# Kernel optimization log

Measured on AMD Instinct MI355X. Metric: run time of the kernel, lower is better.

Reference implementation:

```python
import jax, jax.numpy as jnp
import numpy as np

N, E = 100000, 1600000
NFEAT, NHID, NCLASS = 128, 128, 40


def _glorot(key, shape):
    lim = float(np.sqrt(6.0 / (shape[0] + shape[1])))
    return jax.random.uniform(key, shape, jnp.float32, -lim, lim)


def setup_inputs() -> dict:
    key = jax.random.key(0)
    ks = jax.random.split(key, 9)
    x = jax.random.normal(ks[0], (N, NFEAT), jnp.float32)
    edge_index = jax.random.randint(ks[1], (2, E), 0, N, jnp.int32)
    return {
        "x": x,
        "edge_index": edge_index,
        # layer 1: lin_l (aggregated, with bias) and lin_r (root, no bias)
        "W1l": _glorot(ks[2], (NFEAT, NHID)), "b1": jnp.zeros((NHID,), jnp.float32),
        "W1r": _glorot(ks[3], (NFEAT, NHID)),
        "W2l": _glorot(ks[4], (NHID, NHID)), "b2": jnp.zeros((NHID,), jnp.float32),
        "W2r": _glorot(ks[5], (NHID, NHID)),
        "W3l": _glorot(ks[6], (NHID, NCLASS)), "b3": jnp.zeros((NCLASS,), jnp.float32),
        "W3r": _glorot(ks[7], (NHID, NCLASS)),
    }


def _sage_conv(x, src, dst, Wl, bl, Wr):
    # mean-aggregate source features at destination nodes (PyG SAGEConv, aggr='mean')
    msg = x[src]                                                  # [E, d] gather
    agg = jax.ops.segment_sum(msg, dst, num_segments=N)           # [N, d] scatter-add
    deg = jax.ops.segment_sum(jnp.ones((src.shape[0], 1), x.dtype), dst, num_segments=N)
    mean = agg / jnp.maximum(deg, 1.0)
    return mean @ Wl + bl + x @ Wr


def reference(x, edge_index, W1l, b1, W1r, W2l, b2, W2r, W3l, b3, W3r):
    src, dst = edge_index[0], edge_index[1]
    h = jax.nn.relu(_sage_conv(x, src, dst, W1l, b1, W1r))
    # dropout is identity in eval mode (training=False)
    h = jax.nn.relu(_sage_conv(h, src, dst, W2l, b2, W2r))
    embeddings = h
    logits = _sage_conv(h, src, dst, W3l, b3, W3r)
    return jax.nn.log_softmax(logits, axis=1), embeddings
```

## Files before the change

kernel.cpp:

```cpp
#include <hip/hip_runtime.h>
#include <math.h>

#define NCLASS 40
#define BEDG 1024
#define CAP 24576

typedef float f32x4 __attribute__((ext_vector_type(4)));
typedef __bf16 bf16x8 __attribute__((ext_vector_type(8)));

typedef __attribute__((address_space(1))) const void gv_t;
typedef __attribute__((address_space(3))) void lv_t;
#define GLOAD_LDS16(g, l) __builtin_amdgcn_global_load_lds((gv_t*)(g), (lv_t*)(l), 16, 0, 0)
#define NTL(p) __builtin_nontemporal_load(p)

__device__ inline unsigned short f2bf(float f) {
  unsigned u = __float_as_uint(f);
  unsigned r = (u + 0x7fff + ((u >> 16) & 1)) >> 16;
  return (unsigned short)r;
}
__device__ inline float bflo(unsigned v) { return __uint_as_float(v << 16); }
__device__ inline float bfhi(unsigned v) { return __uint_as_float(v & 0xffff0000u); }


__global__ void k_bcount(const int* __restrict__ dst, int E, int PART,
                         int* __restrict__ bcnt) {
  __shared__ int lc[8];
  int k = blockIdx.x;
  if (threadIdx.x < 8) lc[threadIdx.x] = 0;
  __syncthreads();
  int lo = k * BEDG, hi = min(lo + BEDG, E);
  for (int i = lo + threadIdx.x; i < hi; i += blockDim.x)
    atomicAdd(&lc[NTL(&dst[i]) / PART], 1);
  __syncthreads();
  if (threadIdx.x < 8) bcnt[k * 8 + threadIdx.x] = lc[threadIdx.x];
}

__global__ void k_bscanA(int* __restrict__ bcnt, int nbB, int* __restrict__ btot) {
  __shared__ int tmp[256];
  __shared__ int carryS;
  int b = blockIdx.x;
  int tid = threadIdx.x;
  if (tid == 0) carryS = 0;
  __syncthreads();
  for (int c0 = 0; c0 < nbB; c0 += 256) {
    int idx = c0 + tid;
    int v = (idx < nbB) ? bcnt[idx * 8 + b] : 0;
    tmp[tid] = v;
    __syncthreads();
    for (int d = 1; d < 256; d <<= 1) {
      int t = (tid >= d) ? tmp[tid - d] : 0;
      __syncthreads();
      tmp[tid] += t;
      __syncthreads();
    }
    if (idx < nbB) bcnt[idx * 8 + b] = carryS + tmp[tid] - v;
    __syncthreads();
    if (tid == 255) carryS += tmp[255];
    __syncthreads();
  }
  if (tid == 0) btot[b] = carryS;
}

__global__ void k_bbase(const int* __restrict__ btot, int* __restrict__ bbase) {
  if (threadIdx.x == 0) {
    int s = 0;
    for (int b = 0; b < 8; ++b) {
      bbase[b] = s;
      s += btot[b];
    }
    bbase[8] = s;
  }
}

__global__ void k_place(const int* __restrict__ dst, const int* __restrict__ src, int E,
                        int PART, const int* __restrict__ bcnt,
                        const int* __restrict__ bbase, int* __restrict__ ebuf) {
  __shared__ int lbase[8];
  __shared__ int lcnt[8];
  int k = blockIdx.x;
  if (threadIdx.x < 8) {
    lbase[threadIdx.x] = bbase[threadIdx.x] + bcnt[k * 8 + threadIdx.x];
    lcnt[threadIdx.x] = 0;
  }
  __syncthreads();
  int lo = k * BEDG, hi = min(lo + BEDG, E);
  for (int i = lo + threadIdx.x; i < hi; i += blockDim.x) {
    int d = NTL(&dst[i]);
    int s = NTL(&src[i]);
    int p = d / PART;
    int r = atomicAdd(&lcnt[p], 1);
    ebuf[lbase[p] + r] = (int)(((unsigned)(d - p * PART) << 17) | (unsigned)s);
  }
}

__global__ void k_bcount2(const int* __restrict__ ebuf, const int* __restrict__ bbase,
                          int CB, int* __restrict__ bcnt2) {
  __shared__ int lc[32];
  int p = blockIdx.x & 7, j = blockIdx.x >> 3;
  int tid = threadIdx.x;
  if (tid < 32) lc[tid] = 0;
  __syncthreads();
  int lo = bbase[p], hi = bbase[p + 1];
  for (int base = lo + j * BEDG; base < hi; base += CB * BEDG) {
    int end = min(base + BEDG, hi);
    for (int i = base + tid; i < end; i += 256)
      atomicAdd(&lc[(((unsigned)NTL(&ebuf[i])) >> 17) >> 9], 1);
  }
  __syncthreads();
  if (tid < 32) bcnt2[(p * CB + j) * 32 + tid] = lc[tid];
}

__global__ void k_bscan2(int* __restrict__ bcnt2, int CB, int* __restrict__ tot2) {
  __shared__ int tmp[256];
  int p = blockIdx.x >> 5, k = blockIdx.x & 31;
  int tid = threadIdx.x;
  int v = (tid < CB) ? bcnt2[(p * CB + tid) * 32 + k] : 0;
  tmp[tid] = v;
  __syncthreads();
  for (int d = 1; d < 256; d <<= 1) {
    int t = (tid >= d) ? tmp[tid - d] : 0;
    __syncthreads();
    tmp[tid] += t;
    __syncthreads();
  }
  if (tid < CB) bcnt2[(p * CB + tid) * 32 + k] = tmp[tid] - v;
  if (tid == 255) tot2[p * 32 + k] = tmp[255];
}

__global__ void k_base2(const int* __restrict__ bbase, const int* __restrict__ tot2,
                        int* __restrict__ base2) {
  int p = threadIdx.x;
  if (p >= 8) return;
  int s = bbase[p];
  for (int k = 0; k < 32; ++k) {
    base2[p * 32 + k] = s;
    s += tot2[p * 32 + k];
  }
}

__global__ void k_place2(const int* __restrict__ ebuf, const int* __restrict__ bbase,
                         const int* __restrict__ bcnt2, const int* __restrict__ base2,
                         int CB, int* __restrict__ ebuf2) {
  __shared__ int lb[32];
  int p = blockIdx.x & 7, j = blockIdx.x >> 3;
  int tid = threadIdx.x;
  if (tid < 32) lb[tid] = base2[p * 32 + tid] + bcnt2[(p * CB + j) * 32 + tid];
  __syncthreads();
  int lo = bbase[p], hi = bbase[p + 1];
  for (int base = lo + j * BEDG; base < hi; base += CB * BEDG) {
    int end = min(base + BEDG, hi);
    for (int i = base + tid; i < end; i += 256) {
      unsigned pk = (unsigned)NTL(&ebuf[i]);
      int pos = atomicAdd(&lb[(pk >> 17) >> 9], 1);
      ebuf2[pos] = (int)pk;
    }
  }
}

__global__ __launch_bounds__(256) void k_csr(const int* __restrict__ ebuf2,
                                             const int* __restrict__ base2,
                                             const int* __restrict__ tot2, int PART,
                                             int N, int E, int* __restrict__ off,
                                             int* __restrict__ col) {
  __shared__ int cnt[512];
  __shared__ int cur[512];
  __shared__ int tmp[256];
  __shared__ int stage[CAP];
  int p = blockIdx.x & 7, k = blockIdx.x >> 3;
  int tid = threadIdx.x;
  if (p == 0 && k == 0 && tid == 0) off[N] = E;
  int n0l = k << 9;
  if (n0l >= PART) return;
  int node0 = p * PART + n0l;
  if (node0 >= N) return;
  int nn = min(512, PART - n0l);
  nn = min(nn, N - node0);
  int lo = base2[p * 32 + k];
  int tot = tot2[p * 32 + k];

  cnt[tid] = 0;
  cnt[tid + 256] = 0;
  __syncthreads();
  for (int i = lo + tid; i < lo + tot; i += 256)
    atomicAdd(&cnt[(((unsigned)ebuf2[i]) >> 17) & 511], 1);
  __syncthreads();

  int v0 = cnt[2 * tid], v1 = cnt[2 * tid + 1];
  int s = v0 + v1;
  tmp[tid] = s;
  __syncthreads();
  for (int d = 1; d < 256; d <<= 1) {
    int t = (tid >= d) ? tmp[tid - d] : 0;
    __syncthreads();
    tmp[tid] += t;
    __syncthreads();
  }
  int excl = tmp[tid] - s;
  cnt[2 * tid] = excl;
  cnt[2 * tid + 1] = excl + v0;
  cur[2 * tid] = excl;
  cur[2 * tid + 1] = excl + v0;
  __syncthreads();

  for (int i = tid; i < nn; i += 256) off[node0 + i] = lo + cnt[i];

  if (tot <= CAP) {
    for (int i = lo + tid; i < lo + tot; i += 256) {
      unsigned pk = (unsigned)ebuf2[i];
      int pos = atomicAdd(&cur[(pk >> 17) & 511], 1);
      stage[pos] = (int)(pk & 0x1FFFFu);
    }
    __syncthreads();
    for (int i = tid; i < tot; i += 256) col[lo + i] = stage[i];
  } else {
    for (int i = lo + tid; i < lo + tot; i += 256) {
      unsigned pk = (unsigned)ebuf2[i];
      int pos = atomicAdd(&cur[(pk >> 17) & 511], 1);
      col[lo + pos] = (int)(pk & 0x1FFFFu);
    }
  }
}

__global__ void k_cast(const float4* __restrict__ x, uint4* __restrict__ xb, int n8) {
  int i = blockIdx.x * blockDim.x + threadIdx.x;
  if (i >= n8) return;
  float4 a = x[i * 2], b = x[i * 2 + 1];
  uint4 o;
  o.x = (unsigned)f2bf(a.x) | ((unsigned)f2bf(a.y) << 16);
  o.y = (unsigned)f2bf(a.z) | ((unsigned)f2bf(a.w) << 16);
  o.z = (unsigned)f2bf(b.x) | ((unsigned)f2bf(b.y) << 16);
  o.w = (unsigned)f2bf(b.z) | ((unsigned)f2bf(b.w) << 16);
  xb[i] = o;
}

__global__ void k_prepw(const float* __restrict__ W1l, const float* __restrict__ W1r,
                        const float* __restrict__ W2l, const float* __restrict__ W2r,
                        const float* __restrict__ W3l, const float* __restrict__ W3r,
                        unsigned short* __restrict__ Wth1, unsigned short* __restrict__ Wth2,
                        unsigned short* __restrict__ Wth3) {
  int idx = blockIdx.x * blockDim.x + threadIdx.x;
  if (idx < 32768) {
    int h = idx >> 14, c = (idx >> 7) & 127, k = idx & 127;
    const float* W = h ? W1r : W1l;
    Wth1[idx] = f2bf(W[k * 128 + c]);
  } else if (idx < 65536) {
    int j = idx - 32768;
    int h = j >> 14, c = (j >> 7) & 127, k = j & 127;
    const float* W = h ? W2r : W2l;
    Wth2[j] = f2bf(W[k * 128 + c]);
  } else if (idx < 65536 + 16384) {
    int j = idx - 65536;
    int h = j >> 13, c = (j >> 7) & 63, k = j & 127;
    float v = 0.f;
    if (c < NCLASS) v = (h ? W3r : W3l)[k * NCLASS + c];
    Wth3[j] = f2bf(v);
  }
}

#define ACC8(u, sc)                          \
  acc[0] = fmaf(bflo(u.x), sc, acc[0]);      \
  acc[1] = fmaf(bfhi(u.x), sc, acc[1]);      \
  acc[2] = fmaf(bflo(u.y), sc, acc[2]);      \
  acc[3] = fmaf(bfhi(u.y), sc, acc[3]);      \
  acc[4] = fmaf(bflo(u.z), sc, acc[4]);      \
  acc[5] = fmaf(bfhi(u.z), sc, acc[5]);      \
  acc[6] = fmaf(bflo(u.w), sc, acc[6]);      \
  acc[7] = fmaf(bfhi(u.w), sc, acc[7]);

__global__ void k_aggb(const char* __restrict__ X, const int* __restrict__ off,
                       const int* __restrict__ col, int n, uint4* __restrict__ out) {
  int wid = (blockIdx.x * blockDim.x + threadIdx.x) >> 6;
  int lane = threadIdx.x & 63;
  if (wid >= n) return;
  int g = lane >> 4, q = lane & 15;
  unsigned qb = (unsigned)q << 4;
  int s = off[wid], e = off[wid + 1];
  float acc[8];
#pragma unroll
  for (int t = 0; t < 8; ++t) acc[t] = 0.f;
  int e1 = e - 1;
  for (int j = s; j < e; j += 8) {
    int i0 = j + g, i1 = i0 + 4;
    int c0 = NTL(&col[min(i0, e1)]);
    int c1 = NTL(&col[min(i1, e1)]);
    float s0 = (i0 < e) ? 1.f : 0.f;
    float s1 = (i1 < e) ? 1.f : 0.f;
    uint4 u0 = *(const uint4*)(X + (((unsigned)c0 << 8) + qb));
    uint4 u1 = *(const uint4*)(X + (((unsigned)c1 << 8) + qb));
    ACC8(u0, s0);
    ACC8(u1, s1);
  }
#pragma unroll
  for (int t = 0; t < 8; ++t) {
    acc[t] += __shfl_xor(acc[t], 16);
    acc[t] += __shfl_xor(acc[t], 32);
  }
  float inv = 1.0f / fmaxf((float)(e - s), 1.0f);
  uint4 o;
  o.x = (unsigned)f2bf(acc[0] * inv) | ((unsigned)f2bf(acc[1] * inv) << 16);
  o.y = (unsigned)f2bf(acc[2] * inv) | ((unsigned)f2bf(acc[3] * inv) << 16);
  o.z = (unsigned)f2bf(acc[4] * inv) | ((unsigned)f2bf(acc[5] * inv) << 16);
  o.w = (unsigned)f2bf(acc[6] * inv) | ((unsigned)f2bf(acc[7] * inv) << 16);
  if (lane < 16) out[(size_t)wid * 16 + lane] = o;
}

template <int COLS, int HALVES, int EPI>
__global__ __launch_bounds__(256) void k_gemm_mfma(
    const unsigned short* __restrict__ Aagg, const unsigned short* __restrict__ Aroot,
    const unsigned short* __restrict__ Wth, const float* __restrict__ bias, int n,
    float* __restrict__ outF, unsigned short* __restrict__ outB) {
  constexpr int RF = 4;
  constexpr int CF = 4;
  __shared__ unsigned short aS[128 * 128];
  __shared__ unsigned short wS[COLS * 128];
  int tid = threadIdx.x;
  int w = tid >> 6, lane = tid & 63, l15 = lane & 15, kg = lane >> 4;
  int rowBase = blockIdx.x * 128;
  int r0 = (w >> 1) * 64;
  int c0 = (w & 1) * 64;

  f32x4 acc[RF][CF];
#pragma unroll
  for (int i = 0; i < RF; ++i)
#pragma unroll
    for (int j = 0; j < CF; ++j) acc[i][j] = (f32x4){0.f, 0.f, 0.f, 0.f};

#pragma unroll
  for (int half = 0; half < HALVES; ++half) {
    if (half) __syncthreads();
    {
      const unsigned short* As = half ? Aroot : Aagg;
#pragma unroll
      for (int it = 0; it < 8; ++it) {
        int row = it * 16 + (tid >> 4);
        int g = rowBase + row;
        g = (g < n) ? g : (n - 1);
        int cb = (tid & 15) << 4;
        int sb = cb ^ ((row & 7) << 4);
        const char* src = (const char*)(As + (size_t)g * 128) + sb;
        char* dst = (char*)aS + it * 4096 + (tid >> 6) * 1024;
        GLOAD_LDS16(src, dst);
      }
      const unsigned short* Ws = Wth + (size_t)half * COLS * 128;
#pragma unroll
      for (int it = 0; it < COLS / 16; ++it) {
        int c = it * 16 + (tid >> 4);
        int cb = (tid & 15) << 4;
        int sb = cb ^ ((c & 7) << 4);
        const char* src = (const char*)(Ws + (size_t)c * 128) + sb;
        char* dst = (char*)wS + it * 4096 + (tid >> 6) * 1024;
        GLOAD_LDS16(src, dst);
      }
      asm volatile("s_waitcnt vmcnt(0)" ::: "memory");
      __syncthreads();
    }
#pragma unroll
    for (int ks = 0; ks < 4; ++ks) {
      int kb = ks * 64 + kg * 16;
      bf16x8 av[RF], bv[CF];
#pragma unroll
      for (int i = 0; i < RF; ++i) {
        int row = r0 + i * 16 + l15;
        av[i] = *(const bf16x8*)((const char*)aS + row * 256 + (kb ^ ((row & 7) << 4)));
      }
#pragma unroll
      for (int j = 0; j < CF; ++j) {
        int c = c0 + j * 16 + l15;
        bv[j] = *(const bf16x8*)((const char*)wS + c * 256 + (kb ^ ((c & 7) << 4)));
      }
#pragma unroll
      for (int i = 0; i < RF; ++i)
#pragma unroll
        for (int j = 0; j < CF; ++j)
          acc[i][j] = __builtin_amdgcn_mfma_f32_16x16x32_bf16(av[i], bv[j], acc[i][j], 0, 0, 0);
    }
  }

  if (EPI == 3) {
    bool leftHalf = (c0 == 0);
    unsigned short* R3b = (unsigned short*)outF;
    float bcol[CF];
#pragma unroll
    for (int j = 0; j < CF; ++j) {
      int c = c0 + j * 16 + l15;
      bcol[j] = (!leftHalf && (c - 64) < NCLASS) ? bias[c - 64] : 0.f;
    }
#pragma unroll
    for (int i = 0; i < RF; ++i) {
#pragma unroll
      for (int r = 0; r < 4; ++r) {
        int row = rowBase + r0 + i * 16 + kg * 4 + r;
        if (row >= n) continue;
#pragma unroll
        for (int j = 0; j < CF; ++j) {
          int c = c0 + j * 16 + l15;
          if (leftHalf) {
            outB[(size_t)row * 64 + c] = f2bf(acc[i][j][r]);
          } else {
            R3b[(size_t)row * 64 + (c - 64)] = f2bf(acc[i][j][r] + bcol[j]);
          }
        }
      }
    }
  } else {
    float bcol[CF];
#pragma unroll
    for (int j = 0; j < CF; ++j) bcol[j] = bias[c0 + j * 16 + l15];
#pragma unroll
    for (int i = 0; i < RF; ++i) {
#pragma unroll
      for (int r = 0; r < 4; ++r) {
        int row = rowBase + r0 + i * 16 + kg * 4 + r;
        if (row >= n) continue;
#pragma unroll
        for (int j = 0; j < CF; ++j) {
          float v = fmaxf(acc[i][j][r] + bcol[j], 0.f);
          int c = c0 + j * 16 + l15;
          outB[(size_t)row * 128 + c] = f2bf(v);
          if (EPI == 1) outF[(size_t)row * 128 + c] = v;
        }
      }
    }
  }
}

__global__ void k_agg3ls(const char* __restrict__ Y3, const char* __restrict__ R3,
                         const int* __restrict__ off, const int* __restrict__ col, int n,
                         float* __restrict__ out) {
  int wid = (blockIdx.x * blockDim.x + threadIdx.x) >> 6;
  int lane = threadIdx.x & 63;
  if (wid >= n) return;
  int g = lane >> 3, q = lane & 7;
  unsigned qb = (unsigned)q << 4;
  int s = off[wid], e = off[wid + 1];
  float acc[8];
#pragma unroll
  for (int t = 0; t < 8; ++t) acc[t] = 0.f;
  int e1 = e - 1;
  for (int j = s; j < e; j += 16) {
    int i0 = j + g, i1 = i0 + 8;
    int c0 = NTL(&col[min(i0, e1)]);
    int c1 = NTL(&col[min(i1, e1)]);
    float s0 = (i0 < e) ? 1.f : 0.f;
    float s1 = (i1 < e) ? 1.f : 0.f;
    uint4 u0 = *(const uint4*)(Y3 + (((unsigned)c0 << 7) + qb));
    uint4 u1 = *(const uint4*)(Y3 + (((unsigned)c1 << 7) + qb));
    ACC8(u0, s0);
    ACC8(u1, s1);
  }
#pragma unroll
  for (int t = 0; t < 8; ++t) {
    acc[t] += __shfl_xor(acc[t], 8);
    acc[t] += __shfl_xor(acc[t], 16);
    acc[t] += __shfl_xor(acc[t], 32);
  }
  float inv = 1.0f / fmaxf((float)(e - s), 1.0f);
  uint4 ur = *(const uint4*)(R3 + (((unsigned)wid << 7) + qb));
  float v[8];
  v[0] = acc[0] * inv + bflo(ur.x);
  v[1] = acc[1] * inv + bfhi(ur.x);
  v[2] = acc[2] * inv + bflo(ur.y);
  v[3] = acc[3] * inv + bfhi(ur.y);
  v[4] = acc[4] * inv + bflo(ur.z);
  v[5] = acc[5] * inv + bfhi(ur.z);
  v[6] = acc[6] * inv + bflo(ur.w);
  v[7] = acc[7] * inv + bfhi(ur.w);
  bool valid = q < 5;
  float m = -INFINITY;
  if (valid) {
#pragma unroll
    for (int t = 0; t < 8; ++t) m = fmaxf(m, v[t]);
  }
  m = fmaxf(m, __shfl_xor(m, 1));
  m = fmaxf(m, __shfl_xor(m, 2));
  m = fmaxf(m, __shfl_xor(m, 4));
  float sum = 0.f;
  if (valid) {
#pragma unroll
    for (int t = 0; t < 8; ++t) sum += expf(v[t] - m);
  }
  sum += __shfl_xor(sum, 1);
  sum += __shfl_xor(sum, 2);
  sum += __shfl_xor(sum, 4);
  float ls = logf(sum);
  if (lane < 5) {
    float4 o0 = make_float4(v[0] - m - ls, v[1] - m - ls, v[2] - m - ls, v[3] - m - ls);
    float4 o1 = make_float4(v[4] - m - ls, v[5] - m - ls, v[6] - m - ls, v[7] - m - ls);
    float* op = out + (size_t)wid * NCLASS + lane * 8;
    *(float4*)op = o0;
    *(float4*)(op + 4) = o1;
  }
}

extern "C" void kernel_launch(void* const* d_in, const int* in_sizes, int n_in,
                              void* d_out, int out_size, void* d_ws, size_t ws_size,
                              hipStream_t stream) {
  const float* x = (const float*)d_in[0];
  const int* ei = (const int*)d_in[1];
  const float* W1l = (const float*)d_in[2];
  const float* b1 = (const float*)d_in[3];
  const float* W1r = (const float*)d_in[4];
  const float* W2l = (const float*)d_in[5];
  const float* b2 = (const float*)d_in[6];
  const float* W2r = (const float*)d_in[7];
  const float* W3l = (const float*)d_in[8];
  const float* b3 = (const float*)d_in[9];
  const float* W3r = (const float*)d_in[10];

  int N = in_sizes[0] / 128;
  int E = in_sizes[1] / 2;
  const int* src = ei;
  const int* dst = ei + E;
  int PART = (N + 7) / 8;
  int nbB = (E + BEDG - 1) / BEDG;
  int CB = (E + 8 * BEDG - 1) / (8 * BEDG);
  if (CB > 256) CB = 256;
  if (CB < 1) CB = 1;

  char* wptr = (char*)d_ws;
  auto alloc = [&](size_t bytes) {
    void* p = (void*)wptr;
    wptr += (bytes + 255) & ~(size_t)255;
    return p;
  };
  int* off = (int*)alloc((size_t)(N + 1) * 4);
  int* col = (int*)alloc((size_t)E * 4);
  int* bcnt = (int*)alloc((size_t)nbB * 8 * 4);
  int* btot = (int*)alloc(16 * 4);
  int* bbase = (int*)alloc(16 * 4);
  int* bcnt2 = (int*)alloc((size_t)8 * CB * 32 * 4);
  int* tot2 = (int*)alloc(256 * 4);
  int* base2 = (int*)alloc(256 * 4);
  unsigned short* Wth1 = (unsigned short*)alloc(32768 * 2);
  unsigned short* Wth2 = (unsigned short*)alloc(32768 * 2);
  unsigned short* Wth3 = (unsigned short*)alloc(16384 * 2);
  unsigned short* xb = (unsigned short*)alloc((size_t)N * 128 * 2);
  unsigned short* mb = (unsigned short*)alloc((size_t)N * 128 * 2);
  unsigned short* h1 = (unsigned short*)alloc((size_t)N * 128 * 2);
  unsigned short* h2 = (unsigned short*)alloc((size_t)N * 128 * 2);

  float* outLS = (float*)d_out;
  float* emb = (float*)d_out + (size_t)N * NCLASS;

  int* ebuf = (int*)h2;
  int* ebuf2 = (int*)h2 + E;
  unsigned short* Y3 = mb;
  unsigned short* R3b = h1;

  k_bcount<<<nbB, 256, 0, stream>>>(dst, E, PART, bcnt);
  k_bscanA<<<8, 256, 0, stream>>>(bcnt, nbB, btot);
  k_bbase<<<1, 64, 0, stream>>>(btot, bbase);
  k_place<<<nbB, 256, 0, stream>>>(dst, src, E, PART, bcnt, bbase, ebuf);
  k_bcount2<<<8 * CB, 256, 0, stream>>>(ebuf, bbase, CB, bcnt2);
  k_bscan2<<<256, 256, 0, stream>>>(bcnt2, CB, tot2);
  k_base2<<<1, 64, 0, stream>>>(bbase, tot2, base2);
  k_place2<<<8 * CB, 256, 0, stream>>>(ebuf, bbase, bcnt2, base2, CB, ebuf2);
  k_csr<<<256, 256, 0, stream>>>(ebuf2, base2, tot2, PART, N, E, off, col);

  int n8 = N * 16;
  k_cast<<<(n8 + 255) / 256, 256, 0, stream>>>((const float4*)x, (uint4*)xb, n8);
  k_prepw<<<(81920 + 255) / 256, 256, 0, stream>>>(W1l, W1r, W2l, W2r, W3l, W3r, Wth1,
                                                   Wth2, Wth3);

  int ab = (N * 64 + 255) / 256;
  int gb = (N + 127) / 128;

  k_aggb<<<ab, 256, 0, stream>>>((const char*)xb, off, col, N, (uint4*)mb);
  k_gemm_mfma<128, 2, 0><<<gb, 256, 0, stream>>>(mb, xb, Wth1, b1, N, nullptr, h1);
  k_aggb<<<ab, 256, 0, stream>>>((const char*)h1, off, col, N, (uint4*)mb);
  k_gemm_mfma<128, 2, 1><<<gb, 256, 0, stream>>>(mb, h1, Wth2, b2, N, emb, h2);
  k_gemm_mfma<128, 1, 3><<<gb, 256, 0, stream>>>(h2, nullptr, Wth3, b3, N, (float*)R3b, Y3);
  k_agg3ls<<<ab, 256, 0, stream>>>((const char*)Y3, (const char*)R3b, off, col, N, outLS);
}
```

Baseline: 313.9 us.

## Gather neighbor features in FP8 and simplify CSR build to one-pass bucket sort

Layer 1 and layer 2 neighbor aggregation now read FP8 copies of the node features. The input cast and the layer-1 GEMM epilogue write these copies, so gather bandwidth is roughly halved compared with bf16. Each wave also processes 16 edges per iteration instead of 8. The CSR construction drops the two-level 8-partition bucketing and goes straight to 512-node superblocks, which removes several kernel launches and one full pass over the edges. The cost is a large precision loss in the aggregated features from FP8 e4m3, and extra writes for the FP8 buffers.

```diff
diff --git a/kernel.cpp b/kernel.cpp
--- a/kernel.cpp
+++ b/kernel.cpp
@@ -2,10 +2,11 @@
 #include <math.h>
 
 #define NCLASS 40
-#define BEDG 1024
+#define BEDG4 4096
 #define CAP 24576
 
 typedef float f32x4 __attribute__((ext_vector_type(4)));
+typedef float f32x2 __attribute__((ext_vector_type(2)));
 typedef __bf16 bf16x8 __attribute__((ext_vector_type(8)));
 
 typedef __attribute__((address_space(1))) const void gv_t;
@@ -21,21 +22,43 @@
 __device__ inline float bflo(unsigned v) { return __uint_as_float(v << 16); }
 __device__ inline float bfhi(unsigned v) { return __uint_as_float(v & 0xffff0000u); }
 
-
-__global__ void k_bcount(const int* __restrict__ dst, int E, int PART,
-                         int* __restrict__ bcnt) {
-  __shared__ int lc[8];
+#define ACCQ(u, sc)                                                                  \
+  do {                                                                               \
+    f32x2 p_;                                                                        \
+    p_ = __builtin_amdgcn_cvt_pk_f32_fp8(u.x, false);                                \
+    acc[0] = fmaf(p_.x, sc, acc[0]); acc[1] = fmaf(p_.y, sc, acc[1]);                \
+    p_ = __builtin_amdgcn_cvt_pk_f32_fp8(u.x, true);                                 \
+    acc[2] = fmaf(p_.x, sc, acc[2]); acc[3] = fmaf(p_.y, sc, acc[3]);                \
+    p_ = __builtin_amdgcn_cvt_pk_f32_fp8(u.y, false);                                \
+    acc[4] = fmaf(p_.x, sc, acc[4]); acc[5] = fmaf(p_.y, sc, acc[5]);                \
+    p_ = __builtin_amdgcn_cvt_pk_f32_fp8(u.y, true);                                 \
+    acc[6] = fmaf(p_.x, sc, acc[6]); acc[7] = fmaf(p_.y, sc, acc[7]);                \
+    p_ = __builtin_amdgcn_cvt_pk_f32_fp8(u.z, false);                                \
+    acc[8] = fmaf(p_.x, sc, acc[8]); acc[9] = fmaf(p_.y, sc, acc[9]);                \
+    p_ = __builtin_amdgcn_cvt_pk_f32_fp8(u.z, true);                                 \
+    acc[10] = fmaf(p_.x, sc, acc[10]); acc[11] = fmaf(p_.y, sc, acc[11]);            \
+    p_ = __builtin_amdgcn_cvt_pk_f32_fp8(u.w, false);                                \
+    acc[12] = fmaf(p_.x, sc, acc[12]); acc[13] = fmaf(p_.y, sc, acc[13]);            \
+    p_ = __builtin_amdgcn_cvt_pk_f32_fp8(u.w, true);                                 \
+    acc[14] = fmaf(p_.x, sc, acc[14]); acc[15] = fmaf(p_.y, sc, acc[15]);            \
+  } while (0)
+
+
+__global__ __launch_bounds__(256) void k_bcountF(const int* __restrict__ dst, int E,
+                                                 int* __restrict__ bcnt) {
+  __shared__ int lc[256];
   int k = blockIdx.x;
-  if (threadIdx.x < 8) lc[threadIdx.x] = 0;
-  __syncthreads();
-  int lo = k * BEDG, hi = min(lo + BEDG, E);
-  for (int i = lo + threadIdx.x; i < hi; i += blockDim.x)
-    atomicAdd(&lc[NTL(&dst[i]) / PART], 1);
-  __syncthreads();
-  if (threadIdx.x < 8) bcnt[k * 8 + threadIdx.x] = lc[threadIdx.x];
-}
-
-__global__ void k_bscanA(int* __restrict__ bcnt, int nbB, int* __restrict__ btot) {
+  int tid = threadIdx.x;
+  lc[tid] = 0;
+  __syncthreads();
+  int lo = k * BEDG4, hi = min(lo + BEDG4, E);
+  for (int i = lo + tid; i < hi; i += 256) atomicAdd(&lc[NTL(&dst[i]) >> 9], 1);
+  __syncthreads();
+  bcnt[k * 256 + tid] = lc[tid];
+}
+
+__global__ __launch_bounds__(256) void k_bscanF(int* __restrict__ bcnt, int nbB,
+                                                int* __restrict__ tot) {
   __shared__ int tmp[256];
   __shared__ int carryS;
   int b = blockIdx.x;
@@ -44,7 +67,7 @@
   __syncthreads();
   for (int c0 = 0; c0 < nbB; c0 += 256) {
     int idx = c0 + tid;
-    int v = (idx < nbB) ? bcnt[idx * 8 + b] : 0;
+    int v = (idx < nbB) ? bcnt[idx * 256 + b] : 0;
     tmp[tid] = v;
     __syncthreads();
     for (int d = 1; d < 256; d <<= 1) {
@@ -53,135 +76,75 @@
       tmp[tid] += t;
       __syncthreads();
     }
-    if (idx < nbB) bcnt[idx * 8 + b] = carryS + tmp[tid] - v;
+    if (idx < nbB) bcnt[idx * 256 + b] = carryS + tmp[tid] - v;
     __syncthreads();
     if (tid == 255) carryS += tmp[255];
     __syncthreads();
   }
-  if (tid == 0) btot[b] = carryS;
-}
-
-__global__ void k_bbase(const int* __restrict__ btot, int* __restrict__ bbase) {
-  if (threadIdx.x == 0) {
-    int s = 0;
-    for (int b = 0; b < 8; ++b) {
-      bbase[b] = s;
-      s += btot[b];
-    }
-    bbase[8] = s;
-  }
-}
-
-__global__ void k_place(const int* __restrict__ dst, const int* __restrict__ src, int E,
-                        int PART, const int* __restrict__ bcnt,
-                        const int* __restrict__ bbase, int* __restrict__ ebuf) {
-  __shared__ int lbase[8];
-  __shared__ int lcnt[8];
+  if (tid == 0) tot[b] = carryS;
+}
+
+__global__ __launch_bounds__(256) void k_baseF(const int* __restrict__ tot, int NSB,
+                                               int N, int E, int* __restrict__ base2,
+                                               int* __restrict__ off) {
+  __shared__ int tmp[256];
+  int tid = threadIdx.x;
+  int v = (tid < NSB) ? tot[tid] : 0;
+  tmp[tid] = v;
+  __syncthreads();
+  for (int d = 1; d < 256; d <<= 1) {
+    int t = (tid >= d) ? tmp[tid - d] : 0;
+    __syncthreads();
+    tmp[tid] += t;
+    __syncthreads();
+  }
+  base2[tid] = tmp[tid] - v;
+  if (tid == 0) {
+    base2[NSB] = E;
+    off[N] = E;
+  }
+}
+
+__global__ __launch_bounds__(256) void k_placeF(const int* __restrict__ dst,
+                                                const int* __restrict__ src, int E,
+                                                const int* __restrict__ bcnt,
+                                                const int* __restrict__ base2,
+                                                int* __restrict__ ebuf2) {
+  __shared__ int lb[256];
   int k = blockIdx.x;
-  if (threadIdx.x < 8) {
-    lbase[threadIdx.x] = bbase[threadIdx.x] + bcnt[k * 8 + threadIdx.x];
-    lcnt[threadIdx.x] = 0;
-  }
-  __syncthreads();
-  int lo = k * BEDG, hi = min(lo + BEDG, E);
-  for (int i = lo + threadIdx.x; i < hi; i += blockDim.x) {
+  int tid = threadIdx.x;
+  lb[tid] = base2[tid] + bcnt[k * 256 + tid];
+  __syncthreads();
+  int lo = k * BEDG4, hi = min(lo + BEDG4, E);
+  for (int i = lo + tid; i < hi; i += 256) {
     int d = NTL(&dst[i]);
     int s = NTL(&src[i]);
-    int p = d / PART;
-    int r = atomicAdd(&lcnt[p], 1);
-    ebuf[lbase[p] + r] = (int)(((unsigned)(d - p * PART) << 17) | (unsigned)s);
-  }
-}
-
-__global__ void k_bcount2(const int* __restrict__ ebuf, const int* __restrict__ bbase,
-                          int CB, int* __restrict__ bcnt2) {
-  __shared__ int lc[32];
-  int p = blockIdx.x & 7, j = blockIdx.x >> 3;
-  int tid = threadIdx.x;
-  if (tid < 32) lc[tid] = 0;
-  __syncthreads();
-  int lo = bbase[p], hi = bbase[p + 1];
-  for (int base = lo + j * BEDG; base < hi; base += CB * BEDG) {
-    int end = min(base + BEDG, hi);
-    for (int i = base + tid; i < end; i += 256)
-      atomicAdd(&lc[(((unsigned)NTL(&ebuf[i])) >> 17) >> 9], 1);
-  }
-  __syncthreads();
-  if (tid < 32) bcnt2[(p * CB + j) * 32 + tid] = lc[tid];
-}
-
-__global__ void k_bscan2(int* __restrict__ bcnt2, int CB, int* __restrict__ tot2) {
-  __shared__ int tmp[256];
-  int p = blockIdx.x >> 5, k = blockIdx.x & 31;
-  int tid = threadIdx.x;
-  int v = (tid < CB) ? bcnt2[(p * CB + tid) * 32 + k] : 0;
-  tmp[tid] = v;
-  __syncthreads();
-  for (int d = 1; d < 256; d <<= 1) {
-    int t = (tid >= d) ? tmp[tid - d] : 0;
-    __syncthreads();
-    tmp[tid] += t;
-    __syncthreads();
-  }
-  if (tid < CB) bcnt2[(p * CB + tid) * 32 + k] = tmp[tid] - v;
-  if (tid == 255) tot2[p * 32 + k] = tmp[255];
-}
-
-__global__ void k_base2(const int* __restrict__ bbase, const int* __restrict__ tot2,
-                        int* __restrict__ base2) {
-  int p = threadIdx.x;
-  if (p >= 8) return;
-  int s = bbase[p];
-  for (int k = 0; k < 32; ++k) {
-    base2[p * 32 + k] = s;
-    s += tot2[p * 32 + k];
-  }
-}
-
-__global__ void k_place2(const int* __restrict__ ebuf, const int* __restrict__ bbase,
-                         const int* __restrict__ bcnt2, const int* __restrict__ base2,
-                         int CB, int* __restrict__ ebuf2) {
-  __shared__ int lb[32];
-  int p = blockIdx.x & 7, j = blockIdx.x >> 3;
-  int tid = threadIdx.x;
-  if (tid < 32) lb[tid] = base2[p * 32 + tid] + bcnt2[(p * CB + j) * 32 + tid];
-  __syncthreads();
-  int lo = bbase[p], hi = bbase[p + 1];
-  for (int base = lo + j * BEDG; base < hi; base += CB * BEDG) {
-    int end = min(base + BEDG, hi);
-    for (int i = base + tid; i < end; i += 256) {
-      unsigned pk = (unsigned)NTL(&ebuf[i]);
-      int pos = atomicAdd(&lb[(pk >> 17) >> 9], 1);
-      ebuf2[pos] = (int)pk;
-    }
-  }
-}
-
-__global__ __launch_bounds__(256) void k_csr(const int* __restrict__ ebuf2,
-                                             const int* __restrict__ base2,
-                                             const int* __restrict__ tot2, int PART,
-                                             int N, int E, int* __restrict__ off,
-                                             int* __restrict__ col) {
+    int pos = atomicAdd(&lb[d >> 9], 1);
+    ebuf2[pos] = (int)(((unsigned)(d & 511) << 17) | (unsigned)s);
+  }
+}
+
+__global__ __launch_bounds__(256) void k_csrF(const int* __restrict__ ebuf2,
+                                              const int* __restrict__ base2,
+                                              const int* __restrict__ tot, int N,
+                                              int* __restrict__ off,
+                                              int* __restrict__ col) {
   __shared__ int cnt[512];
   __shared__ int cur[512];
   __shared__ int tmp[256];
   __shared__ int stage[CAP];
-  int p = blockIdx.x & 7, k = blockIdx.x >> 3;
+  int sb = blockIdx.x;
   int tid = threadIdx.x;
-  if (p == 0 && k == 0 && tid == 0) off[N] = E;
-  int n0l = k << 9;
-  if (n0l >= PART) return;
-  int node0 = p * PART + n0l;
+  int node0 = sb << 9;
   if (node0 >= N) return;
-  int nn = min(512, PART - n0l);
-  nn = min(nn, N - node0);
-  int lo = base2[p * 32 + k];
-  int tot = tot2[p * 32 + k];
+  int nn = min(512, N - node0);
+  int lo = base2[sb];
+  int t2 = tot[sb];
 
   cnt[tid] = 0;
   cnt[tid + 256] = 0;
   __syncthreads();
-  for (int i = lo + tid; i < lo + tot; i += 256)
+  for (int i = lo + tid; i < lo + t2; i += 256)
     atomicAdd(&cnt[(((unsigned)ebuf2[i]) >> 17) & 511], 1);
   __syncthreads();
 
@@ -204,16 +167,16 @@
 
   for (int i = tid; i < nn; i += 256) off[node0 + i] = lo + cnt[i];
 
-  if (tot <= CAP) {
-    for (int i = lo + tid; i < lo + tot; i += 256) {
+  if (t2 <= CAP) {
+    for (int i = lo + tid; i < lo + t2; i += 256) {
       unsigned pk = (unsigned)ebuf2[i];
       int pos = atomicAdd(&cur[(pk >> 17) & 511], 1);
       stage[pos] = (int)(pk & 0x1FFFFu);
     }
     __syncthreads();
-    for (int i = tid; i < tot; i += 256) col[lo + i] = stage[i];
+    for (int i = tid; i < t2; i += 256) col[lo + i] = stage[i];
   } else {
-    for (int i = lo + tid; i < lo + tot; i += 256) {
+    for (int i = lo + tid; i < lo + t2; i += 256) {
       unsigned pk = (unsigned)ebuf2[i];
       int pos = atomicAdd(&cur[(pk >> 17) & 511], 1);
       col[lo + pos] = (int)(pk & 0x1FFFFu);
@@ -221,7 +184,8 @@
   }
 }
 
-__global__ void k_cast(const float4* __restrict__ x, uint4* __restrict__ xb, int n8) {
+__global__ void k_cast(const float4* __restrict__ x, uint4* __restrict__ xb,
+                       uint2* __restrict__ xq, int n8) {
   int i = blockIdx.x * blockDim.x + threadIdx.x;
   if (i >= n8) return;
   float4 a = x[i * 2], b = x[i * 2 + 1];
@@ -231,6 +195,11 @@
   o.z = (unsigned)f2bf(b.x) | ((unsigned)f2bf(b.y) << 16);
   o.w = (unsigned)f2bf(b.z) | ((unsigned)f2bf(b.w) << 16);
   xb[i] = o;
+  unsigned lo = __builtin_amdgcn_cvt_pk_fp8_f32(a.x, a.y, 0, false);
+  lo = __builtin_amdgcn_cvt_pk_fp8_f32(a.z, a.w, lo, true);
+  unsigned hi = __builtin_amdgcn_cvt_pk_fp8_f32(b.x, b.y, 0, false);
+  hi = __builtin_amdgcn_cvt_pk_fp8_f32(b.z, b.w, hi, true);
+  xq[i] = make_uint2(lo, hi);
 }
 
 __global__ void k_prepw(const float* __restrict__ W1l, const float* __restrict__ W1r,
@@ -257,51 +226,49 @@
   }
 }
 
-#define ACC8(u, sc)                          \
-  acc[0] = fmaf(bflo(u.x), sc, acc[0]);      \
-  acc[1] = fmaf(bfhi(u.x), sc, acc[1]);      \
-  acc[2] = fmaf(bflo(u.y), sc, acc[2]);      \
-  acc[3] = fmaf(bfhi(u.y), sc, acc[3]);      \
-  acc[4] = fmaf(bflo(u.z), sc, acc[4]);      \
-  acc[5] = fmaf(bfhi(u.z), sc, acc[5]);      \
-  acc[6] = fmaf(bflo(u.w), sc, acc[6]);      \
-  acc[7] = fmaf(bfhi(u.w), sc, acc[7]);
-
-__global__ void k_aggb(const char* __restrict__ X, const int* __restrict__ off,
+__global__ void k_aggq(const char* __restrict__ Xq, const int* __restrict__ off,
                        const int* __restrict__ col, int n, uint4* __restrict__ out) {
   int wid = (blockIdx.x * blockDim.x + threadIdx.x) >> 6;
   int lane = threadIdx.x & 63;
   if (wid >= n) return;
-  int g = lane >> 4, q = lane & 15;
+  int g = lane >> 3, q = lane & 7;
   unsigned qb = (unsigned)q << 4;
   int s = off[wid], e = off[wid + 1];
-  float acc[8];
-#pragma unroll
-  for (int t = 0; t < 8; ++t) acc[t] = 0.f;
+  float acc[16];
+#pragma unroll
+  for (int t = 0; t < 16; ++t) acc[t] = 0.f;
   int e1 = e - 1;
-  for (int j = s; j < e; j += 8) {
-    int i0 = j + g, i1 = i0 + 4;
+  for (int j = s; j < e; j += 16) {
+    int i0 = j + g, i1 = i0 + 8;
     int c0 = NTL(&col[min(i0, e1)]);
     int c1 = NTL(&col[min(i1, e1)]);
     float s0 = (i0 < e) ? 1.f : 0.f;
     float s1 = (i1 < e) ? 1.f : 0.f;
-    uint4 u0 = *(const uint4*)(X + (((unsigned)c0 << 8) + qb));
-    uint4 u1 = *(const uint4*)(X + (((unsigned)c1 << 8) + qb));
-    ACC8(u0, s0);
-    ACC8(u1, s1);
-  }
-#pragma unroll
-  for (int t = 0; t < 8; ++t) {
+    uint4 u0 = *(const uint4*)(Xq + (((unsigned)c0 << 7) + qb));
+    uint4 u1 = *(const uint4*)(Xq + (((unsigned)c1 << 7) + qb));
+    ACCQ(u0, s0);
+    ACCQ(u1, s1);
+  }
+#pragma unroll
+  for (int t = 0; t < 16; ++t) {
+    acc[t] += __shfl_xor(acc[t], 8);
     acc[t] += __shfl_xor(acc[t], 16);
     acc[t] += __shfl_xor(acc[t], 32);
   }
   float inv = 1.0f / fmaxf((float)(e - s), 1.0f);
-  uint4 o;
-  o.x = (unsigned)f2bf(acc[0] * inv) | ((unsigned)f2bf(acc[1] * inv) << 16);
-  o.y = (unsigned)f2bf(acc[2] * inv) | ((unsigned)f2bf(acc[3] * inv) << 16);
-  o.z = (unsigned)f2bf(acc[4] * inv) | ((unsigned)f2bf(acc[5] * inv) << 16);
-  o.w = (unsigned)f2bf(acc[6] * inv) | ((unsigned)f2bf(acc[7] * inv) << 16);
-  if (lane < 16) out[(size_t)wid * 16 + lane] = o;
+  if (lane < 8) {
+    uint4 o0, o1;
+    o0.x = (unsigned)f2bf(acc[0] * inv) | ((unsigned)f2bf(acc[1] * inv) << 16);
+    o0.y = (unsigned)f2bf(acc[2] * inv) | ((unsigned)f2bf(acc[3] * inv) << 16);
+    o0.z = (unsigned)f2bf(acc[4] * inv) | ((unsigned)f2bf(acc[5] * inv) << 16);
+    o0.w = (unsigned)f2bf(acc[6] * inv) | ((unsigned)f2bf(acc[7] * inv) << 16);
+    o1.x = (unsigned)f2bf(acc[8] * inv) | ((unsigned)f2bf(acc[9] * inv) << 16);
+    o1.y = (unsigned)f2bf(acc[10] * inv) | ((unsigned)f2bf(acc[11] * inv) << 16);
+    o1.z = (unsigned)f2bf(acc[12] * inv) | ((unsigned)f2bf(acc[13] * inv) << 16);
+    o1.w = (unsigned)f2bf(acc[14] * inv) | ((unsigned)f2bf(acc[15] * inv) << 16);
+    out[(size_t)wid * 16 + q * 2] = o0;
+    out[(size_t)wid * 16 + q * 2 + 1] = o1;
+  }
 }
 
 template <int COLS, int HALVES, int EPI>
@@ -418,11 +385,25 @@
           int c = c0 + j * 16 + l15;
           outB[(size_t)row * 128 + c] = f2bf(v);
           if (EPI == 1) outF[(size_t)row * 128 + c] = v;
+          if (EPI == 0) {
+            unsigned pk = __builtin_amdgcn_cvt_pk_fp8_f32(v, v, 0, false);
+            ((unsigned char*)outF)[(size_t)row * 128 + c] = (unsigned char)(pk & 0xff);
+          }
         }
       }
     }
   }
 }
+
+#define ACC8(u, sc)                          \
+  acc[0] = fmaf(bflo(u.x), sc, acc[0]);      \
+  acc[1] = fmaf(bfhi(u.x), sc, acc[1]);      \
+  acc[2] = fmaf(bflo(u.y), sc, acc[2]);      \
+  acc[3] = fmaf(bfhi(u.y), sc, acc[3]);      \
+  acc[4] = fmaf(bflo(u.z), sc, acc[4]);      \
+  acc[5] = fmaf(bfhi(u.z), sc, acc[5]);      \
+  acc[6] = fmaf(bflo(u.w), sc, acc[6]);      \
+  acc[7] = fmaf(bfhi(u.w), sc, acc[7]);
 
 __global__ void k_agg3ls(const char* __restrict__ Y3, const char* __restrict__ R3,
                          const int* __restrict__ off, const int* __restrict__ col, int n,
@@ -457,14 +438,14 @@
   float inv = 1.0f / fmaxf((float)(e - s), 1.0f);
   uint4 ur = *(const uint4*)(R3 + (((unsigned)wid << 7) + qb));
   float v[8];
-  v[0] = acc[0] * inv + bflo(ur.x);
-  v[1] = acc[1] * inv + bfhi(ur.x);
-  v[2] = acc[2] * inv + bflo(ur.y);
-  v[3] = acc[3] * inv + bfhi(ur.y);
-  v[4] = acc[4] * inv + bflo(ur.z);
-  v[5] = acc[5] * inv + bfhi(ur.z);
-  v[6] = acc[6] * inv + bflo(ur.w);
-  v[7] = acc[7] * inv + bfhi(ur.w);
+  v[0] = fmaf(acc[0], inv, bflo(ur.x));
+  v[1] = fmaf(acc[1], inv, bfhi(ur.x));
+  v[2] = fmaf(acc[2], inv, bflo(ur.y));
+  v[3] = fmaf(acc[3], inv, bfhi(ur.y));
+  v[4] = fmaf(acc[4], inv, bflo(ur.z));
+  v[5] = fmaf(acc[5], inv, bfhi(ur.z));
+  v[6] = fmaf(acc[6], inv, bflo(ur.w));
+  v[7] = fmaf(acc[7], inv, bfhi(ur.w));
   bool valid = q < 5;
   float m = -INFINITY;
   if (valid) {
@@ -511,11 +492,8 @@
   int E = in_sizes[1] / 2;
   const int* src = ei;
   const int* dst = ei + E;
-  int PART = (N + 7) / 8;
-  int nbB = (E + BEDG - 1) / BEDG;
-  int CB = (E + 8 * BEDG - 1) / (8 * BEDG);
-  if (CB > 256) CB = 256;
-  if (CB < 1) CB = 1;
+  int NSB = (N + 511) >> 9;
+  int nbB = (E + BEDG4 - 1) / BEDG4;
 
   char* wptr = (char*)d_ws;
   auto alloc = [&](size_t bytes) {
@@ -525,12 +503,9 @@
   };
   int* off = (int*)alloc((size_t)(N + 1) * 4);
   int* col = (int*)alloc((size_t)E * 4);
-  int* bcnt = (int*)alloc((size_t)nbB * 8 * 4);
-  int* btot = (int*)alloc(16 * 4);
-  int* bbase = (int*)alloc(16 * 4);
-  int* bcnt2 = (int*)alloc((size_t)8 * CB * 32 * 4);
-  int* tot2 = (int*)alloc(256 * 4);
-  int* base2 = (int*)alloc(256 * 4);
+  int* bcnt = (int*)alloc((size_t)nbB * 256 * 4);
+  int* tot = (int*)alloc(256 * 4);
+  int* base2 = (int*)alloc(257 * 4);
   unsigned short* Wth1 = (unsigned short*)alloc(32768 * 2);
   unsigned short* Wth2 = (unsigned short*)alloc(32768 * 2);
   unsigned short* Wth3 = (unsigned short*)alloc(16384 * 2);
@@ -538,36 +513,34 @@
   unsigned short* mb = (unsigned short*)alloc((size_t)N * 128 * 2);
   unsigned short* h1 = (unsigned short*)alloc((size_t)N * 128 * 2);
   unsigned short* h2 = (unsigned short*)alloc((size_t)N * 128 * 2);
+  unsigned char* xq = (unsigned char*)alloc((size_t)N * 128);
+  unsigned char* h1q = (unsigned char*)alloc((size_t)N * 128);
 
   float* outLS = (float*)d_out;
   float* emb = (float*)d_out + (size_t)N * NCLASS;
 
-  int* ebuf = (int*)h2;
-  int* ebuf2 = (int*)h2 + E;
+  int* ebuf2 = (int*)h2;
   unsigned short* Y3 = mb;
   unsigned short* R3b = h1;
 
-  k_bcount<<<nbB, 256, 0, stream>>>(dst, E, PART, bcnt);
-  k_bscanA<<<8, 256, 0, stream>>>(bcnt, nbB, btot);
-  k_bbase<<<1, 64, 0, stream>>>(btot, bbase);
-  k_place<<<nbB, 256, 0, stream>>>(dst, src, E, PART, bcnt, bbase, ebuf);
-  k_bcount2<<<8 * CB, 256, 0, stream>>>(ebuf, bbase, CB, bcnt2);
-  k_bscan2<<<256, 256, 0, stream>>>(bcnt2, CB, tot2);
-  k_base2<<<1, 64, 0, stream>>>(bbase, tot2, base2);
-  k_place2<<<8 * CB, 256, 0, stream>>>(ebuf, bbase, bcnt2, base2, CB, ebuf2);
-  k_csr<<<256, 256, 0, stream>>>(ebuf2, base2, tot2, PART, N, E, off, col);
+  k_bcountF<<<nbB, 256, 0, stream>>>(dst, E, bcnt);
+  k_bscanF<<<NSB, 256, 0, stream>>>(bcnt, nbB, tot);
+  k_baseF<<<1, 256, 0, stream>>>(tot, NSB, N, E, base2, off);
+  k_placeF<<<nbB, 256, 0, stream>>>(dst, src, E, bcnt, base2, ebuf2);
+  k_csrF<<<NSB, 256, 0, stream>>>(ebuf2, base2, tot, N, off, col);
 
   int n8 = N * 16;
-  k_cast<<<(n8 + 255) / 256, 256, 0, stream>>>((const float4*)x, (uint4*)xb, n8);
+  k_cast<<<(n8 + 255) / 256, 256, 0, stream>>>((const float4*)x, (uint4*)xb, (uint2*)xq,
+                                               n8);
   k_prepw<<<(81920 + 255) / 256, 256, 0, stream>>>(W1l, W1r, W2l, W2r, W3l, W3r, Wth1,
                                                    Wth2, Wth3);
 
   int ab = (N * 64 + 255) / 256;
   int gb = (N + 127) / 128;
 
-  k_aggb<<<ab, 256, 0, stream>>>((const char*)xb, off, col, N, (uint4*)mb);
-  k_gemm_mfma<128, 2, 0><<<gb, 256, 0, stream>>>(mb, xb, Wth1, b1, N, nullptr, h1);
-  k_aggb<<<ab, 256, 0, stream>>>((const char*)h1, off, col, N, (uint4*)mb);
+  k_aggq<<<ab, 256, 0, stream>>>((const char*)xq, off, col, N, (uint4*)mb);
+  k_gemm_mfma<128, 2, 0><<<gb, 256, 0, stream>>>(mb, xb, Wth1, b1, N, (float*)h1q, h1);
+  k_aggq<<<ab, 256, 0, stream>>>((const char*)h1q, off, col, N, (uint4*)mb);
   k_gemm_mfma<128, 2, 1><<<gb, 256, 0, stream>>>(mb, h1, Wth2, b2, N, emb, h2);
   k_gemm_mfma<128, 1, 3><<<gb, 256, 0, stream>>>(h2, nullptr, Wth3, b3, N, (float*)R3b, Y3);
   k_agg3ls<<<ab, 256, 0, stream>>>((const char*)Y3, (const char*)R3b, off, col, N, outLS);
```

Result: faster. 303.1 us (-3.5%).
